# Optimization experiments

Measured on AMD Instinct MI355X. Metric: run time of the kernel, lower is better.

## Reference

```python
import jax, jax.numpy as jnp
import numpy as np

N_SC, N_AG, N_STEP, HID, N_LAYER = 32, 128, 64, 128, 3


def setup_inputs() -> dict:
    key = jax.random.key(0)
    ks = jax.random.split(key, 6)
    scale = 1.0 / np.sqrt(HID)
    x = jax.random.normal(ks[0], (N_SC, N_AG, N_STEP, HID), dtype=jnp.float32)
    invalid = jax.random.bernoulli(ks[1], 0.1, (N_SC, N_AG, N_STEP))
    w_ih = jax.random.uniform(ks[2], (N_LAYER, 3 * HID, HID), jnp.float32, -scale, scale)
    w_hh = jax.random.uniform(ks[3], (N_LAYER, 3 * HID, HID), jnp.float32, -scale, scale)
    b_ih = jax.random.uniform(ks[4], (N_LAYER, 3 * HID), jnp.float32, -scale, scale)
    b_hh = jax.random.uniform(ks[5], (N_LAYER, 3 * HID), jnp.float32, -scale, scale)
    return {"x": x, "invalid": invalid, "w_ih": w_ih, "w_hh": w_hh, "b_ih": b_ih, "b_hh": b_hh}


def _gru_cell(xt, h, Wi, Wh, bi, bh):
    # torch gate order: r, z, n. xt/h: [B,H]; Wi/Wh: [3H,H]
    gi = xt @ Wi.T + bi
    gh = h @ Wh.T + bh
    ir, iz, i_n = jnp.split(gi, 3, axis=-1)
    hr, hz, h_n = jnp.split(gh, 3, axis=-1)
    r = jax.nn.sigmoid(ir + hr)
    z = jax.nn.sigmoid(iz + hz)
    n = jnp.tanh(i_n + r * h_n)
    return (1.0 - z) * n + z * h


def reference(x, invalid, w_ih, w_hh, b_ih, b_hh):
    n_sc, n_ag, n_step, hd = x.shape
    n_layer = w_ih.shape[0]
    B = n_sc * n_ag
    xs = x.transpose(2, 0, 1, 3).reshape(n_step, B, hd)       # [T,B,H]
    inv = invalid.transpose(2, 0, 1).reshape(n_step, B)[..., None]  # [T,B,1] bool
    h0 = jnp.zeros((n_layer, B, hd), x.dtype)

    def step(h, inp):
        xt, mt = inp  # [B,H], [B,1]
        out = xt
        hs = []
        for l in range(n_layer):  # small fixed layer count
            hl = _gru_cell(out, h[l], w_ih[l], w_hh[l], b_ih[l], b_hh[l])
            hs.append(hl)
            out = hl
        h_new = jnp.where(mt[None], 0.0, jnp.stack(hs))  # masked hidden reset, all layers
        y = jnp.where(mt, 0.0, out)                      # masked output
        return h_new, y

    _, ys = jax.lax.scan(step, h0, (xs, inv))  # ys: [T,B,H]
    x_1 = ys.reshape(n_step, n_sc, n_ag, hd).transpose(1, 2, 0, 3)
    return x_1
```

## Files before the change

### kernel.cpp

```cpp
#include <hip/hip_runtime.h>
#include <hip/hip_bf16.h>


#define T_STEPS 64
#define HID 128
#define NL 3
#define RB 16
#define NTHR 512
#define NBLK 256
#define LSTR 136

typedef __attribute__((ext_vector_type(8))) short bf16x8;
typedef __attribute__((ext_vector_type(4))) short short4v;
typedef __attribute__((ext_vector_type(4))) float f32x4;

static __device__ __forceinline__ short f2bf_s(float f) {
  __hip_bfloat16 b = __float2bfloat16(f);
  return __builtin_bit_cast(short, b);
}
static __device__ __forceinline__ float rcp_f(float x) {
  float r; asm("v_rcp_f32 %0, %1" : "=v"(r) : "v"(x)); return r;
}
static __device__ __forceinline__ float exp2_f(float x) {
  float r; asm("v_exp_f32 %0, %1" : "=v"(r) : "v"(x)); return r;
}

#define MFMA(A, B, C) __builtin_amdgcn_mfma_f32_16x16x32_bf16((A), (B), (C), 0, 0, 0)

#define NL2E  (-1.4426950408889634f)
#define T2L2E (2.8853900817779268f)

template <bool SRCBF, bool LASTL>
__device__ __forceinline__ void layer_pass(
    const float* __restrict__ wih, const float* __restrict__ whh,
    const float* __restrict__ bih, const float* __restrict__ bhh,
    const float* srcf, const unsigned short* srcb,
    float* dstf, unsigned short* dstb,
    unsigned mw0, unsigned mw1,
    short (*s_x)[RB * LSTR], short (*s_h)[RB * LSTR],
    int tid, int wave, int lr, int lq, int srow, int scol, int cb)
{
  bf16x8 wI[3][4], wH[3][4];
#pragma unroll
  for (int g = 0; g < 3; ++g) {
    const float sc = (g < 2) ? NL2E : T2L2E;
#pragma unroll
    for (int kf = 0; kf < 4; ++kf) {
      const int wrow = g * HID + wave * 16 + lr;
      const int kofs = kf * 32 + lq * 8;
      const float* pI = wih + (size_t)wrow * HID + kofs;
      const float* pH = whh + (size_t)wrow * HID + kofs;
      float4 a = *(const float4*)pI, b = *(const float4*)(pI + 4);
      float vi[8] = {a.x, a.y, a.z, a.w, b.x, b.y, b.z, b.w};
      float4 c = *(const float4*)pH, d = *(const float4*)(pH + 4);
      float vh[8] = {c.x, c.y, c.z, c.w, d.x, d.y, d.z, d.w};
#pragma unroll
      for (int j = 0; j < 8; ++j) {
        wI[g][kf][j] = f2bf_s(sc * vi[j]);
        wH[g][kf][j] = f2bf_s(sc * vh[j]);
      }
    }
  }
  f32x4 bRZ0v, bRZ1v, bNiv, bNhv;
#pragma unroll
  for (int ri = 0; ri < 4; ++ri) {
    const int c = cb + ri;
    bRZ0v[ri] = NL2E * (bih[c] + bhh[c]);
    bRZ1v[ri] = NL2E * (bih[HID + c] + bhh[HID + c]);
    bNiv[ri]  = T2L2E * bih[2 * HID + c];
    bNhv[ri]  = T2L2E * bhh[2 * HID + c];
  }

  for (int i = tid; i < RB * LSTR; i += NTHR) s_h[0][i] = 0;
  if (SRCBF) {
    *(short4v*)&s_x[0][srow * LSTR + scol] = *(const short4v*)srcb;
  } else {
    float4 v = *(const float4*)srcf;
    short4v c4 = {f2bf_s(v.x), f2bf_s(v.y), f2bf_s(v.z), f2bf_s(v.w)};
    *(short4v*)&s_x[0][srow * LSTR + scol] = c4;
  }
  float hprev[4] = {0.f, 0.f, 0.f, 0.f};
  __syncthreads();

  for (int t = 0; t < T_STEPS; ++t) {
    const int p = t & 1;
    float4 pinf;
    short4v pinb;
    if (t < T_STEPS - 1) {
      if (SRCBF) pinb = *(const short4v*)(srcb + (size_t)(t + 1) * HID);
      else       pinf = *(const float4*)(srcf + (size_t)(t + 1) * HID);
    }
    const int mk = (int)((((t & 32) ? mw1 : mw0) >> (t & 31)) & 1u);

    f32x4 aI0 = bRZ0v, aH0 = (f32x4)(0.f);
    f32x4 aI1 = bRZ1v, aH1 = (f32x4)(0.f);
    f32x4 aN = bNiv, aHn = bNhv;
#pragma unroll
    for (int kf = 0; kf < 4; ++kf) {
      const int ao = lr * LSTR + kf * 32 + lq * 8;
      bf16x8 xh = *(const bf16x8*)&s_x[p][ao];
      bf16x8 hh = *(const bf16x8*)&s_h[p][ao];
      aI0 = MFMA(wI[0][kf], xh, aI0);
      aH0 = MFMA(wH[0][kf], hh, aH0);
      aI1 = MFMA(wI[1][kf], xh, aI1);
      aH1 = MFMA(wH[1][kf], hh, aH1);
      aN  = MFMA(wI[2][kf], xh, aN);
      aHn = MFMA(wH[2][kf], hh, aHn);
    }

    float4 actf;
    short4v ab, hb;
#pragma unroll
    for (int ri = 0; ri < 4; ++ri) {
      float rr = rcp_f(1.f + exp2_f(aI0[ri] + aH0[ri]));
      float zz = rcp_f(1.f + exp2_f(aI1[ri] + aH1[ri]));
      float en = exp2_f(fmaf(rr, aHn[ri], aN[ri]));
      float nn = fmaf(-2.f, rcp_f(en + 1.f), 1.f);
      float hn = fmaf(zz, hprev[ri] - nn, nn);
      float hm = mk ? 0.f : hn;
      hprev[ri] = hm;
      short bf = f2bf_s(hn);
      hb[ri] = mk ? (short)0 : bf;
      if (LASTL) ((float*)&actf)[ri] = hm;
      else       ab[ri] = bf;
    }
    if (LASTL) *(float4*)(dstf + (size_t)t * HID) = actf;
    else       *(short4v*)(dstb + (size_t)t * HID) = ab;
    *(short4v*)&s_h[p ^ 1][lr * LSTR + cb] = hb;

    if (t < T_STEPS - 1) {
      if (SRCBF) {
        *(short4v*)&s_x[p ^ 1][srow * LSTR + scol] = pinb;
      } else {
        short4v c4 = {f2bf_s(pinf.x), f2bf_s(pinf.y), f2bf_s(pinf.z), f2bf_s(pinf.w)};
        *(short4v*)&s_x[p ^ 1][srow * LSTR + scol] = c4;
      }
    }
    asm volatile("s_waitcnt lgkmcnt(0)" ::: "memory");
    __builtin_amdgcn_s_barrier();
  }
}

__global__ __launch_bounds__(NTHR, 1) void gru13(
    const float* __restrict__ x, const int* __restrict__ invalid,
    const float* __restrict__ w_ih, const float* __restrict__ w_hh,
    const float* __restrict__ b_ih, const float* __restrict__ b_hh,
    float* out, unsigned short* ws)
{
  __shared__ short s_x[2][RB * LSTR];
  __shared__ short s_h[2][RB * LSTR];
  __shared__ unsigned s_mw[RB * 2];

  const int tid = threadIdx.x;
  const int wave = tid >> 6, lane = tid & 63;
  const int lr = lane & 15, lq = lane >> 4;
  const int row_base = (int)blockIdx.x * RB;
  const int srow = tid >> 5, scol = (tid & 31) * 4;
  const int cb = wave * 16 + lq * 4;

  {
    const int rr = 2 * wave + (lane >> 5);
    const int tt = lane & 31;
    const size_t base = (size_t)(row_base + rr) * T_STEPS;
    unsigned long long b1 = __ballot(invalid[base + tt] != 0);
    unsigned long long b2 = __ballot(invalid[base + 32 + tt] != 0);
    if (lane == 0) {
      s_mw[(2 * wave) * 2]         = (unsigned)b1;
      s_mw[(2 * wave + 1) * 2]     = (unsigned)(b1 >> 32);
      s_mw[(2 * wave) * 2 + 1]     = (unsigned)b2;
      s_mw[(2 * wave + 1) * 2 + 1] = (unsigned)(b2 >> 32);
    }
  }
  __syncthreads();
  const unsigned mw0 = s_mw[lr * 2], mw1 = s_mw[lr * 2 + 1];

  const size_t soff = (size_t)(row_base + srow) * T_STEPS * HID + scol;
  const size_t doff = (size_t)(row_base + lr) * T_STEPS * HID + cb;

  layer_pass<false, false>(w_ih, w_hh, b_ih, b_hh,
                           x + soff, nullptr, nullptr, ws + doff,
                           mw0, mw1, s_x, s_h, tid, wave, lr, lq, srow, scol, cb);
  __syncthreads();
  layer_pass<true, false>(w_ih + 3 * HID * HID, w_hh + 3 * HID * HID,
                          b_ih + 3 * HID, b_hh + 3 * HID,
                          nullptr, ws + soff, nullptr, ws + doff,
                          mw0, mw1, s_x, s_h, tid, wave, lr, lq, srow, scol, cb);
  __syncthreads();
  layer_pass<true, true>(w_ih + 6 * HID * HID, w_hh + 6 * HID * HID,
                         b_ih + 6 * HID, b_hh + 6 * HID,
                         nullptr, ws + soff, out + doff, nullptr,
                         mw0, mw1, s_x, s_h, tid, wave, lr, lq, srow, scol, cb);
}

extern "C" void kernel_launch(void* const* d_in, const int* in_sizes, int n_in,
                              void* d_out, int out_size, void* d_ws, size_t ws_size,
                              hipStream_t stream) {
  const float* x       = (const float*)d_in[0];
  const int*   invalid = (const int*)d_in[1];
  const float* w_ih    = (const float*)d_in[2];
  const float* w_hh    = (const float*)d_in[3];
  const float* b_ih    = (const float*)d_in[4];
  const float* b_hh    = (const float*)d_in[5];
  gru13<<<dim3(NBLK), dim3(NTHR), 0, stream>>>(x, invalid, w_ih, w_hh, b_ih, b_hh,
                                               (float*)d_out, (unsigned short*)d_ws);
}
```

Before: 216.5 us.

## Software-pipeline input-gate MFMAs one step ahead off the recurrence critical path

Computes the input projection (W_ih·x) for step t+1 after the gate math of step t, so each step only issues the hidden-state MFMAs before the nonlinearity. The x staging buffer grows from 2 to 4 LDS slots and input prefetch moves two steps ahead to keep the pipeline fed. This aims to shorten the serial dependency chain per timestep. In exchange it holds three extra accumulator vectors in registers and uses more shared memory.

```diff
diff --git a/kernel.cpp b/kernel.cpp
--- a/kernel.cpp
+++ b/kernel.cpp
@@ -72,39 +72,44 @@
   }
 
   for (int i = tid; i < RB * LSTR; i += NTHR) s_h[0][i] = 0;
-  if (SRCBF) {
-    *(short4v*)&s_x[0][srow * LSTR + scol] = *(const short4v*)srcb;
-  } else {
-    float4 v = *(const float4*)srcf;
-    short4v c4 = {f2bf_s(v.x), f2bf_s(v.y), f2bf_s(v.z), f2bf_s(v.w)};
-    *(short4v*)&s_x[0][srow * LSTR + scol] = c4;
+#pragma unroll
+  for (int st = 0; st < 2; ++st) {
+    if (SRCBF) {
+      *(short4v*)&s_x[st][srow * LSTR + scol] = *(const short4v*)(srcb + (size_t)st * HID);
+    } else {
+      float4 v = *(const float4*)(srcf + (size_t)st * HID);
+      short4v c4 = {f2bf_s(v.x), f2bf_s(v.y), f2bf_s(v.z), f2bf_s(v.w)};
+      *(short4v*)&s_x[st][srow * LSTR + scol] = c4;
+    }
+  }
+  __syncthreads();
+
+  f32x4 gA0 = bRZ0v, gA1 = bRZ1v, gAn = bNiv;
+#pragma unroll
+  for (int kf = 0; kf < 4; ++kf) {
+    bf16x8 xh = *(const bf16x8*)&s_x[0][lr * LSTR + kf * 32 + lq * 8];
+    gA0 = MFMA(wI[0][kf], xh, gA0);
+    gA1 = MFMA(wI[1][kf], xh, gA1);
+    gAn = MFMA(wI[2][kf], xh, gAn);
   }
   float hprev[4] = {0.f, 0.f, 0.f, 0.f};
-  __syncthreads();
 
   for (int t = 0; t < T_STEPS; ++t) {
     const int p = t & 1;
     float4 pinf;
     short4v pinb;
-    if (t < T_STEPS - 1) {
-      if (SRCBF) pinb = *(const short4v*)(srcb + (size_t)(t + 1) * HID);
-      else       pinf = *(const float4*)(srcf + (size_t)(t + 1) * HID);
+    if (t < T_STEPS - 2) {
+      if (SRCBF) pinb = *(const short4v*)(srcb + (size_t)(t + 2) * HID);
+      else       pinf = *(const float4*)(srcf + (size_t)(t + 2) * HID);
     }
     const int mk = (int)((((t & 32) ? mw1 : mw0) >> (t & 31)) & 1u);
 
-    f32x4 aI0 = bRZ0v, aH0 = (f32x4)(0.f);
-    f32x4 aI1 = bRZ1v, aH1 = (f32x4)(0.f);
-    f32x4 aN = bNiv, aHn = bNhv;
+    f32x4 aH0 = (f32x4)(0.f), aH1 = (f32x4)(0.f), aHn = bNhv;
 #pragma unroll
     for (int kf = 0; kf < 4; ++kf) {
-      const int ao = lr * LSTR + kf * 32 + lq * 8;
-      bf16x8 xh = *(const bf16x8*)&s_x[p][ao];
-      bf16x8 hh = *(const bf16x8*)&s_h[p][ao];
-      aI0 = MFMA(wI[0][kf], xh, aI0);
+      bf16x8 hh = *(const bf16x8*)&s_h[p][lr * LSTR + kf * 32 + lq * 8];
       aH0 = MFMA(wH[0][kf], hh, aH0);
-      aI1 = MFMA(wI[1][kf], xh, aI1);
       aH1 = MFMA(wH[1][kf], hh, aH1);
-      aN  = MFMA(wI[2][kf], xh, aN);
       aHn = MFMA(wH[2][kf], hh, aHn);
     }
 
@@ -112,9 +117,9 @@
     short4v ab, hb;
 #pragma unroll
     for (int ri = 0; ri < 4; ++ri) {
-      float rr = rcp_f(1.f + exp2_f(aI0[ri] + aH0[ri]));
-      float zz = rcp_f(1.f + exp2_f(aI1[ri] + aH1[ri]));
-      float en = exp2_f(fmaf(rr, aHn[ri], aN[ri]));
+      float rr = rcp_f(1.f + exp2_f(gA0[ri] + aH0[ri]));
+      float zz = rcp_f(1.f + exp2_f(gA1[ri] + aH1[ri]));
+      float en = exp2_f(fmaf(rr, aHn[ri], gAn[ri]));
       float nn = fmaf(-2.f, rcp_f(en + 1.f), 1.f);
       float hn = fmaf(zz, hprev[ri] - nn, nn);
       float hm = mk ? 0.f : hn;
@@ -124,16 +129,29 @@
       if (LASTL) ((float*)&actf)[ri] = hm;
       else       ab[ri] = bf;
     }
+
+    if (t < T_STEPS - 1) {
+      const short* xb = &s_x[(t + 1) & 3][lr * LSTR + lq * 8];
+      f32x4 n0 = bRZ0v, n1 = bRZ1v, n2 = bNiv;
+#pragma unroll
+      for (int kf = 0; kf < 4; ++kf) {
+        bf16x8 xh = *(const bf16x8*)(xb + kf * 32);
+        n0 = MFMA(wI[0][kf], xh, n0);
+        n1 = MFMA(wI[1][kf], xh, n1);
+        n2 = MFMA(wI[2][kf], xh, n2);
+      }
+      gA0 = n0; gA1 = n1; gAn = n2;
+    }
+
     if (LASTL) *(float4*)(dstf + (size_t)t * HID) = actf;
     else       *(short4v*)(dstb + (size_t)t * HID) = ab;
     *(short4v*)&s_h[p ^ 1][lr * LSTR + cb] = hb;
-
-    if (t < T_STEPS - 1) {
+    if (t < T_STEPS - 2) {
       if (SRCBF) {
-        *(short4v*)&s_x[p ^ 1][srow * LSTR + scol] = pinb;
+        *(short4v*)&s_x[(t + 2) & 3][srow * LSTR + scol] = pinb;
       } else {
         short4v c4 = {f2bf_s(pinf.x), f2bf_s(pinf.y), f2bf_s(pinf.z), f2bf_s(pinf.w)};
-        *(short4v*)&s_x[p ^ 1][srow * LSTR + scol] = c4;
+        *(short4v*)&s_x[(t + 2) & 3][srow * LSTR + scol] = c4;
       }
     }
     asm volatile("s_waitcnt lgkmcnt(0)" ::: "memory");
@@ -141,13 +159,13 @@
   }
 }
 
-__global__ __launch_bounds__(NTHR, 1) void gru13(
+__global__ __launch_bounds__(NTHR, 1) void gru14(
     const float* __restrict__ x, const int* __restrict__ invalid,
     const float* __restrict__ w_ih, const float* __restrict__ w_hh,
     const float* __restrict__ b_ih, const float* __restrict__ b_hh,
     float* out, unsigned short* ws)
 {
-  __shared__ short s_x[2][RB * LSTR];
+  __shared__ short s_x[4][RB * LSTR];
   __shared__ short s_h[2][RB * LSTR];
   __shared__ unsigned s_mw[RB * 2];
 
@@ -201,6 +219,6 @@
   const float* w_hh    = (const float*)d_in[3];
   const float* b_ih    = (const float*)d_in[4];
   const float* b_hh    = (const float*)d_in[5];
-  gru13<<<dim3(NBLK), dim3(NTHR), 0, stream>>>(x, invalid, w_ih, w_hh, b_ih, b_hh,
+  gru14<<<dim3(NBLK), dim3(NTHR), 0, stream>>>(x, invalid, w_ih, w_hh, b_ih, b_hh,
                                                (float*)d_out, (unsigned short*)d_ws);
 }
```

Measured after the change: 213.8 us (median of 2 runs). Within noise of the previous version (-1.3%).
